# Optimization experiments

Measured on AMD Instinct MI355X. Metric: run time of the kernel, lower is better.

## Reference

```python
import jax, jax.numpy as jnp
import numpy as np

T, B, S, D = 128, 32, 100, 256  # targetL, batch, sourceL, output_size
EPS = 1e-6

def setup_inputs() -> dict:
    key = jax.random.key(0)
    ks = jax.random.split(key, 9)
    sc = 0.05  # weight init scale
    inp = {
        'prev_layer': jax.random.normal(ks[0], (T, B, D), dtype=jnp.float32),
        'hidden': jax.random.normal(ks[1], (B, D), dtype=jnp.float32),
        'enc_output': jax.random.normal(ks[2], (T * B, S, D), dtype=jnp.float32),
        # linear weights (layer_norm=True -> no biases on linears)
        'W_in': jax.random.normal(ks[3], (D, 3 * D), dtype=jnp.float32) * sc,
        'W_hid': jax.random.normal(ks[4], (D, D), dtype=jnp.float32) * sc,
        'W_ctx': jax.random.normal(ks[5], (D, D), dtype=jnp.float32) * sc,
        'W_enc': jax.random.normal(ks[6], (D, D), dtype=jnp.float32) * sc,
        'W_q': jax.random.normal(ks[7], (D, D), dtype=jnp.float32) * sc,   # MLPAttention query proj
        'v_att': jax.random.normal(ks[8], (D,), dtype=jnp.float32) * sc,  # MLPAttention score vector
        # layernorm affine params
        'g_pre': jnp.ones(3 * D, jnp.float32), 'b_pre': jnp.zeros(3 * D, jnp.float32),
        'g_enc': jnp.ones(D, jnp.float32), 'b_enc': jnp.zeros(D, jnp.float32),
        'g_h': jnp.ones(D, jnp.float32), 'b_h': jnp.zeros(D, jnp.float32),
        'g_c': jnp.ones(D, jnp.float32), 'b_c': jnp.zeros(D, jnp.float32),
        'g_q': jnp.ones(D, jnp.float32), 'b_q': jnp.zeros(D, jnp.float32),
    }
    return inp

def _ln(x, g, b):
    m = jnp.mean(x, axis=-1, keepdims=True)
    v = jnp.mean((x - m) ** 2, axis=-1, keepdims=True)
    return g * (x - m) / jnp.sqrt(v + EPS) + b

def reference(prev_layer, hidden, enc_output, W_in, W_hid, W_ctx, W_enc, W_q, v_att,
              g_pre, b_pre, g_enc, b_enc, g_h, b_h, g_c, b_c, g_q, b_q):
    Tl, Bb, Dd = prev_layer.shape
    # input / encoder projections (dropout=0 -> identity)
    preact = _ln(prev_layer @ W_in, g_pre, b_pre)        # [T,B,3D]
    pctx = _ln(enc_output @ W_enc, g_enc, b_enc)         # [T*B,S,D]
    z, h_gate, x_t = jnp.split(preact, 3, axis=-1)
    z = jax.nn.sigmoid(z)
    h_gate = jax.nn.sigmoid(h_gate)
    # SRU-style elementwise linear recurrence over time
    def step(h, zx):
        zt, xt = zx
        s = (1.0 - zt) * h + zt * xt
        return s, s
    final_h, ss = jax.lax.scan(step, hidden, (z, x_t))   # ss: [T,B,D]
    # MLP (Bahdanau) attention: scores = v . tanh(LN(Wq s) + pctx)
    q = _ln(ss @ W_q, g_q, b_q).reshape(Tl * Bb, 1, Dd)
    scores = jnp.einsum('nsd,d->ns', jnp.tanh(q + pctx), v_att)  # [T*B,S]
    attn = jax.nn.softmax(scores, axis=-1)
    attn_out = jnp.einsum('ns,nsd->nd', attn, pctx).reshape(Tl, Bb, Dd)
    attn_out = attn_out / np.sqrt(Dd).astype(np.float32)
    out = jnp.tanh(_ln(ss @ W_hid, g_h, b_h) + _ln(attn_out @ W_ctx, g_c, b_c))
    out = (1.0 - h_gate) * out + h_gate * prev_layer     # highway gate
    return out, final_h, attn
```

## Files before the change

### kernel.cpp

```cpp
#include <hip/hip_runtime.h>
#include <hip/hip_bf16.h>
#include <math.h>

typedef short  s16x8 __attribute__((ext_vector_type(8)));
typedef float  f32x4 __attribute__((ext_vector_type(4)));
typedef float  f32x2 __attribute__((ext_vector_type(2)));

#define LN_EPS 1e-6f

__device__ __forceinline__ unsigned short f2bf(float x) {
  union { float f; unsigned u; } v; v.f = x;
  unsigned r = v.u + 0x7FFFu + ((v.u >> 16) & 1u);
  return (unsigned short)(r >> 16);
}
__device__ __forceinline__ float bf2f(unsigned short u) {
  union { unsigned u; float f; } v; v.u = ((unsigned)u) << 16;
  return v.f;
}
__device__ __forceinline__ float bflo(unsigned u) {
  union { unsigned u; float f; } v; v.u = u << 16; return v.f;
}
__device__ __forceinline__ float bfhi(unsigned u) {
  union { unsigned u; float f; } v; v.u = u & 0xFFFF0000u; return v.f;
}
__device__ __forceinline__ unsigned pack_bf2(float a, float b) {
  __hip_bfloat162 h = __float22bfloat162_rn(make_float2(a, b));
  unsigned u; __builtin_memcpy(&u, &h, 4); return u;
}
__device__ __forceinline__ float fast_tanh(float x) {
  float e = __expf(2.0f * x);
  return 1.0f - 2.0f * __builtin_amdgcn_rcpf(e + 1.0f);
}
__device__ __forceinline__ float fast_sigmoid(float x) {
  return __builtin_amdgcn_rcpf(1.0f + __expf(-x));
}

__device__ __forceinline__ float wredsum(float v) {
  #pragma unroll
  for (int m = 32; m >= 1; m >>= 1) v += __shfl_xor(v, m);
  return v;
}

__device__ __forceinline__ f32x4 mfma16(s16x8 a, s16x8 b, f32x4 c) {
  return __builtin_amdgcn_mfma_f32_16x16x32_bf16(a, b, c, 0, 0, 0);
}

__device__ __forceinline__ void stage_rows(unsigned short* A, const float* src,
                                           int rows, int tid, int nthreads) {
  char* Ab = (char*)A;
  int nquads = rows * 64;
  for (int p = tid; p < nquads; p += nthreads) {
    int row = p >> 6, kq = p & 63;
    f32x4 v = *(const f32x4*)(src + row * 256 + kq * 4);
    unsigned u0 = pack_bf2(v.x, v.y);
    unsigned u1 = pack_bf2(v.z, v.w);
    int byte = row * 512 + ((kq * 8) ^ ((row & 7) << 4));
    *(uint2*)(Ab + byte) = uint2{u0, u1};
  }
}

__device__ __forceinline__ s16x8 readA(const unsigned short* A, int row, int kk, int hi) {
  const char* Ab = (const char*)A;
  int byte = row * 512 + (((kk * 64) + hi * 16) ^ ((row & 7) << 4));
  return *(const s16x8*)(Ab + byte);
}
__device__ __forceinline__ s16x8 readB(const unsigned short* Bt, int col, int kk, int hi) {
  return *(const s16x8*)(Bt + col * 256 + kk * 32 + hi * 8);
}

__global__ __launch_bounds__(256) void k_convw(
    const float* Win, const float* Wq, const float* Whid, const float* Wctx, const float* Wenc,
    unsigned short* bt_in, unsigned short* bt_q, unsigned short* bt_hid,
    unsigned short* bt_ctx, unsigned short* bt_enc) {
  int e = blockIdx.x * 256 + threadIdx.x;
  if (e < 196608) {
    int k = e & 255, n = e >> 8;
    bt_in[n * 256 + k] = f2bf(Win[k * 768 + n]);
    return;
  }
  e -= 196608;
  int m = e >> 16;
  int r = e & 65535;
  int k = r & 255, n = r >> 8;
  const float* src = (m == 0) ? Wq : (m == 1) ? Whid : (m == 2) ? Wctx : Wenc;
  unsigned short* dst = (m == 0) ? bt_q : (m == 1) ? bt_hid : (m == 2) ? bt_ctx : bt_enc;
  dst[n * 256 + k] = f2bf(src[k * 256 + n]);
}

__global__ __launch_bounds__(256) void k_preact(
    const float* prev, const unsigned short* bt_in,
    const float* g_pre, const float* b_pre,
    float* Z, float* HG, float* XT) {
  __shared__ __align__(16) unsigned short A[16 * 256];
  __shared__ float C[16 * 768];
  int tid = threadIdx.x, lane = tid & 63, wave = tid >> 6;
  int hi = lane >> 4, lo = lane & 15;
  int r0 = blockIdx.x * 16;
  stage_rows(A, prev + (size_t)r0 * 256, 16, tid, 256);
  __syncthreads();
  f32x4 acc[12];
  #pragma unroll
  for (int ct = 0; ct < 12; ct++) acc[ct] = f32x4{0.f, 0.f, 0.f, 0.f};
  #pragma unroll
  for (int kk = 0; kk < 8; kk++) {
    s16x8 a = readA(A, lo, kk, hi);
    #pragma unroll
    for (int ct = 0; ct < 12; ct++) {
      s16x8 b = readB(bt_in, wave * 192 + ct * 16 + lo, kk, hi);
      acc[ct] = mfma16(a, b, acc[ct]);
    }
  }
  #pragma unroll
  for (int ct = 0; ct < 12; ct++) {
    int col = wave * 192 + ct * 16 + lo;
    #pragma unroll
    for (int r = 0; r < 4; r++) C[(hi * 4 + r) * 768 + col] = acc[ct][r];
  }
  __syncthreads();
  #pragma unroll
  for (int mm = 0; mm < 4; mm++) {
    int m = wave * 4 + mm;
    float x[12]; float s = 0.f, q = 0.f;
    #pragma unroll
    for (int i = 0; i < 12; i++) {
      x[i] = C[m * 768 + lane + 64 * i];
      s += x[i]; q += x[i] * x[i];
    }
    s = wredsum(s); q = wredsum(q);
    float mean = s * (1.0f / 768.0f);
    float var = q * (1.0f / 768.0f) - mean * mean;
    float rstd = rsqrtf(var + LN_EPS);
    int gr = r0 + m;
    #pragma unroll
    for (int i = 0; i < 12; i++) {
      int c = lane + 64 * i;
      float y = g_pre[c] * (x[i] - mean) * rstd + b_pre[c];
      if (c < 256)      Z [gr * 256 + c]         = fast_sigmoid(y);
      else if (c < 512) HG[gr * 256 + (c - 256)] = fast_sigmoid(y);
      else              XT[gr * 256 + (c - 512)] = y;
    }
  }
}

__global__ __launch_bounds__(256) void k_scan(
    const float* hidden, const float* Z, const float* XT,
    float* SS, float* outFinalH) {
  int tid = blockIdx.x * 256 + threadIdx.x;
  float h = hidden[tid];
  for (int t0 = 0; t0 < 128; t0 += 8) {
    float zc[8], xc[8];
    #pragma unroll
    for (int j = 0; j < 8; j++) {
      zc[j] = Z [(t0 + j) * 8192 + tid];
      xc[j] = XT[(t0 + j) * 8192 + tid];
    }
    #pragma unroll
    for (int j = 0; j < 8; j++) {
      h = (1.0f - zc[j]) * h + zc[j] * xc[j];
      SS[(t0 + j) * 8192 + tid] = h;
    }
  }
  outFinalH[tid] = h;
}

__global__ __launch_bounds__(256) void k_qproj(
    const float* SS, const unsigned short* bt_q,
    const float* g_q, const float* b_q, float* Q) {
  __shared__ __align__(16) unsigned short A[16 * 256];
  __shared__ float C[16 * 256];
  int tid = threadIdx.x, lane = tid & 63, wave = tid >> 6;
  int hi = lane >> 4, lo = lane & 15;
  int r0 = blockIdx.x * 16;
  stage_rows(A, SS + (size_t)r0 * 256, 16, tid, 256);
  __syncthreads();
  f32x4 acc[4];
  #pragma unroll
  for (int ct = 0; ct < 4; ct++) acc[ct] = f32x4{0.f, 0.f, 0.f, 0.f};
  #pragma unroll
  for (int kk = 0; kk < 8; kk++) {
    s16x8 a = readA(A, lo, kk, hi);
    #pragma unroll
    for (int ct = 0; ct < 4; ct++) {
      s16x8 b = readB(bt_q, wave * 64 + ct * 16 + lo, kk, hi);
      acc[ct] = mfma16(a, b, acc[ct]);
    }
  }
  #pragma unroll
  for (int ct = 0; ct < 4; ct++) {
    int col = wave * 64 + ct * 16 + lo;
    #pragma unroll
    for (int r = 0; r < 4; r++) C[(hi * 4 + r) * 256 + col] = acc[ct][r];
  }
  __syncthreads();
  #pragma unroll
  for (int mm = 0; mm < 4; mm++) {
    int m = wave * 4 + mm;
    float x[4]; float s = 0.f, q = 0.f;
    #pragma unroll
    for (int i = 0; i < 4; i++) {
      x[i] = C[m * 256 + lane + 64 * i];
      s += x[i]; q += x[i] * x[i];
    }
    s = wredsum(s); q = wredsum(q);
    float mean = s * (1.0f / 256.0f);
    float var = q * (1.0f / 256.0f) - mean * mean;
    float rstd = rsqrtf(var + LN_EPS);
    int gr = r0 + m;
    #pragma unroll
    for (int i = 0; i < 4; i++) {
      int c = lane + 64 * i;
      Q[gr * 256 + c] = g_q[c] * (x[i] - mean) * rstd + b_q[c];
    }
  }
}

__global__ __launch_bounds__(512) void k_attn(
    const float* enc, const unsigned short* bt_enc, const float* Q,
    const float* g_enc, const float* b_enc, const float* v_att,
    float* AOUT, float* attnOut) {
  __shared__ __align__(16) unsigned short AP[112 * 256];
  __shared__ float scores[112];
  __shared__ float beta_s;
  __shared__ float qs[256], gs[256], bs[256], vs[256];
  float*  means = (float*) ((char*)AP + 55296);
  float*  rstds = (float*) ((char*)AP + 55744);
  f32x2*  part  = (f32x2*) ((char*)AP + 51200);
  int n = blockIdx.x;
  int tid = threadIdx.x, lane = tid & 63, wave = tid >> 6;
  int hi = lane >> 4, lo = lane & 15;
  if (tid < 256) {
    qs[tid] = Q[n * 256 + tid];
    gs[tid] = g_enc[tid]; bs[tid] = b_enc[tid]; vs[tid] = v_att[tid];
  }
  stage_rows(AP, enc + (size_t)n * 25600, 100, tid, 512);
  __syncthreads();
  f32x4 acc[7][2];
  #pragma unroll
  for (int mt = 0; mt < 7; mt++) {
    acc[mt][0] = f32x4{0.f, 0.f, 0.f, 0.f};
    acc[mt][1] = f32x4{0.f, 0.f, 0.f, 0.f};
  }
  #pragma unroll
  for (int kk = 0; kk < 8; kk++) {
    s16x8 b0 = readB(bt_enc, wave * 32 + lo, kk, hi);
    s16x8 b1 = readB(bt_enc, wave * 32 + 16 + lo, kk, hi);
    #pragma unroll
    for (int mt = 0; mt < 7; mt++) {
      s16x8 a = readA(AP, mt * 16 + lo, kk, hi);
      acc[mt][0] = mfma16(a, b0, acc[mt][0]);
      acc[mt][1] = mfma16(a, b1, acc[mt][1]);
    }
  }
  __syncthreads();
  #pragma unroll
  for (int mt = 0; mt < 7; mt++) {
    #pragma unroll
    for (int ct = 0; ct < 2; ct++) {
      int col = wave * 32 + ct * 16 + lo;
      #pragma unroll
      for (int r = 0; r < 4; r++) {
        int row = mt * 16 + hi * 4 + r;
        if (row < 100) AP[row * 256 + col] = f2bf(acc[mt][ct][r]);
      }
    }
  }
  __syncthreads();
  {
    int ca = lane * 2;
    float g0 = gs[ca], g1 = gs[ca + 1], g2 = gs[ca + 128], g3 = gs[ca + 129];
    float b0 = bs[ca], b1 = bs[ca + 1], b2 = bs[ca + 128], b3 = bs[ca + 129];
    float v0 = vs[ca], v1 = vs[ca + 1], v2 = vs[ca + 128], v3 = vs[ca + 129];
    float q0 = qs[ca], q1 = qs[ca + 1], q2 = qs[ca + 128], q3 = qs[ca + 129];
    for (int m = wave; m < 100; m += 8) {
      const unsigned* Prow = (const unsigned*)(AP + m * 256);
      unsigned u01 = Prow[lane], u23 = Prow[lane + 64];
      float x0 = bflo(u01), x1 = bfhi(u01), x2 = bflo(u23), x3 = bfhi(u23);
      float s = (x0 + x1) + (x2 + x3);
      float q = fmaf(x0, x0, fmaf(x1, x1, fmaf(x2, x2, x3 * x3)));
      s = wredsum(s); q = wredsum(q);
      float mean = s * (1.0f / 256.0f);
      float var = q * (1.0f / 256.0f) - mean * mean;
      float rstd = rsqrtf(var + LN_EPS);
      float sc;
      sc  = v0 * fast_tanh(q0 + fmaf(g0, (x0 - mean) * rstd, b0));
      sc += v1 * fast_tanh(q1 + fmaf(g1, (x1 - mean) * rstd, b1));
      sc += v2 * fast_tanh(q2 + fmaf(g2, (x2 - mean) * rstd, b2));
      sc += v3 * fast_tanh(q3 + fmaf(g3, (x3 - mean) * rstd, b3));
      sc = wredsum(sc);
      if (lane == 0) { scores[m] = sc; means[m] = mean; rstds[m] = rstd; }
    }
  }
  __syncthreads();
  if (wave == 0) {
    float s1 = (lane < 100) ? scores[lane] : -INFINITY;
    float s2 = (lane + 64 < 100) ? scores[lane + 64] : -INFINITY;
    float mx = fmaxf(s1, s2);
    #pragma unroll
    for (int m = 32; m >= 1; m >>= 1) mx = fmaxf(mx, __shfl_xor(mx, m));
    float e1 = (lane < 100) ? __expf(s1 - mx) : 0.f;
    float e2 = (lane + 64 < 100) ? __expf(s2 - mx) : 0.f;
    float sm = wredsum(e1 + e2);
    float inv = __builtin_amdgcn_rcpf(sm);
    float p1 = e1 * inv, p2 = e2 * inv;
    float r1 = (lane < 100) ? rstds[lane] : 0.f;
    float m1 = (lane < 100) ? means[lane] : 0.f;
    float r2 = (lane + 64 < 100) ? rstds[lane + 64] : 0.f;
    float m2 = (lane + 64 < 100) ? means[lane + 64] : 0.f;
    scores[lane] = p1 * r1;
    if (lane + 64 < 112) scores[lane + 64] = p2 * r2;
    float bp = wredsum(fmaf(p1 * r1, m1, p2 * r2 * m2));
    if (lane == 0) beta_s = bp;
    if (lane < 100) attnOut[(size_t)n * 100 + lane] = p1;
    if (lane + 64 < 100) attnOut[(size_t)n * 100 + lane + 64] = p2;
  }
  __syncthreads();
  {
    int cp = tid & 127, h = tid >> 7;
    float a0 = 0.f, a1 = 0.f;
    #pragma unroll 5
    for (int s = h * 25; s < h * 25 + 25; s++) {
      unsigned u = *(const unsigned*)(AP + s * 256 + cp * 2);
      float al = scores[s];
      a0 = fmaf(al, bflo(u), a0);
      a1 = fmaf(al, bfhi(u), a1);
    }
    part[h * 128 + cp] = f32x2{a0, a1};
  }
  __syncthreads();
  if (tid < 256) {
    const float* pf = (const float*)part;
    int idx = (tid >> 1) * 2 + (tid & 1);
    float S1 = pf[idx] + pf[256 + idx] + pf[512 + idx] + pf[768 + idx];
    float y = fmaf(gs[tid], S1 - beta_s, bs[tid]);
    AOUT[(size_t)n * 256 + tid] = y * 0.0625f;
  }
}

__global__ __launch_bounds__(256) void k_out(
    const float* SS, const float* AOUT,
    const unsigned short* bt_hid, const unsigned short* bt_ctx,
    const float* g_h, const float* b_h, const float* g_c, const float* b_c,
    const float* HG, const float* prev, float* out) {
  __shared__ __align__(16) unsigned short A1[16 * 256];
  __shared__ __align__(16) unsigned short A2[16 * 256];
  __shared__ float C1[16 * 256];
  __shared__ float C2[16 * 256];
  int tid = threadIdx.x, lane = tid & 63, wave = tid >> 6;
  int hi = lane >> 4, lo = lane & 15;
  int r0 = blockIdx.x * 16;
  stage_rows(A1, SS + (size_t)r0 * 256, 16, tid, 256);
  stage_rows(A2, AOUT + (size_t)r0 * 256, 16, tid, 256);
  __syncthreads();
  f32x4 acc1[4], acc2[4];
  #pragma unroll
  for (int ct = 0; ct < 4; ct++) {
    acc1[ct] = f32x4{0.f, 0.f, 0.f, 0.f};
    acc2[ct] = f32x4{0.f, 0.f, 0.f, 0.f};
  }
  #pragma unroll
  for (int kk = 0; kk < 8; kk++) {
    s16x8 a1 = readA(A1, lo, kk, hi);
    s16x8 a2 = readA(A2, lo, kk, hi);
    #pragma unroll
    for (int ct = 0; ct < 4; ct++) {
      int col = wave * 64 + ct * 16 + lo;
      s16x8 b1 = readB(bt_hid, col, kk, hi);
      s16x8 b2 = readB(bt_ctx, col, kk, hi);
      acc1[ct] = mfma16(a1, b1, acc1[ct]);
      acc2[ct] = mfma16(a2, b2, acc2[ct]);
    }
  }
  #pragma unroll
  for (int ct = 0; ct < 4; ct++) {
    int col = wave * 64 + ct * 16 + lo;
    #pragma unroll
    for (int r = 0; r < 4; r++) {
      C1[(hi * 4 + r) * 256 + col] = acc1[ct][r];
      C2[(hi * 4 + r) * 256 + col] = acc2[ct][r];
    }
  }
  __syncthreads();
  #pragma unroll
  for (int mm = 0; mm < 4; mm++) {
    int m = wave * 4 + mm;
    float x1[4], x2[4];
    float s1 = 0.f, q1 = 0.f, s2 = 0.f, q2 = 0.f;
    #pragma unroll
    for (int i = 0; i < 4; i++) {
      x1[i] = C1[m * 256 + lane + 64 * i];
      x2[i] = C2[m * 256 + lane + 64 * i];
      s1 += x1[i]; q1 += x1[i] * x1[i];
      s2 += x2[i]; q2 += x2[i] * x2[i];
    }
    s1 = wredsum(s1); q1 = wredsum(q1);
    s2 = wredsum(s2); q2 = wredsum(q2);
    float mean1 = s1 * (1.0f / 256.0f), var1 = q1 * (1.0f / 256.0f) - mean1 * mean1;
    float mean2 = s2 * (1.0f / 256.0f), var2 = q2 * (1.0f / 256.0f) - mean2 * mean2;
    float rstd1 = rsqrtf(var1 + LN_EPS), rstd2 = rsqrtf(var2 + LN_EPS);
    int gr = r0 + m;
    #pragma unroll
    for (int i = 0; i < 4; i++) {
      int c = lane + 64 * i;
      float y1 = g_h[c] * (x1[i] - mean1) * rstd1 + b_h[c];
      float y2 = g_c[c] * (x2[i] - mean2) * rstd2 + b_c[c];
      float y = fast_tanh(y1 + y2);
      float g = HG[gr * 256 + c];
      float pv = prev[gr * 256 + c];
      out[gr * 256 + c] = (1.0f - g) * y + g * pv;
    }
  }
}

extern "C" void kernel_launch(void* const* d_in, const int* in_sizes, int n_in,
                              void* d_out, int out_size, void* d_ws, size_t ws_size,
                              hipStream_t stream) {
  const float* prev   = (const float*)d_in[0];
  const float* hidden = (const float*)d_in[1];
  const float* enc    = (const float*)d_in[2];
  const float* W_in   = (const float*)d_in[3];
  const float* W_hid  = (const float*)d_in[4];
  const float* W_ctx  = (const float*)d_in[5];
  const float* W_enc  = (const float*)d_in[6];
  const float* W_q    = (const float*)d_in[7];
  const float* v_att  = (const float*)d_in[8];
  const float* g_pre  = (const float*)d_in[9];
  const float* b_pre  = (const float*)d_in[10];
  const float* g_enc  = (const float*)d_in[11];
  const float* b_enc  = (const float*)d_in[12];
  const float* g_h    = (const float*)d_in[13];
  const float* b_h    = (const float*)d_in[14];
  const float* g_c    = (const float*)d_in[15];
  const float* b_c    = (const float*)d_in[16];
  const float* g_q    = (const float*)d_in[17];
  const float* b_q    = (const float*)d_in[18];

  char* ws = (char*)d_ws;
  unsigned short* BT_IN  = (unsigned short*)(ws + 0);
  unsigned short* BT_Q   = (unsigned short*)(ws + 393216);
  unsigned short* BT_HID = (unsigned short*)(ws + 524288);
  unsigned short* BT_CTX = (unsigned short*)(ws + 655360);
  unsigned short* BT_ENC = (unsigned short*)(ws + 786432);
  float* Z    = (float*)(ws + 917504);
  float* HG   = (float*)(ws + 5111808);
  float* XT   = (float*)(ws + 9306112);
  float* SS   = (float*)(ws + 13500416);
  float* Q    = (float*)(ws + 17694720);
  float* AOUT = (float*)(ws + 21889024);

  float* out    = (float*)d_out;
  float* finalH = out + 1048576;
  float* attnO  = out + 1056768;

  k_convw <<<1792, 256, 0, stream>>>(W_in, W_q, W_hid, W_ctx, W_enc,
                                     BT_IN, BT_Q, BT_HID, BT_CTX, BT_ENC);
  k_preact<<<256, 256, 0, stream>>>(prev, BT_IN, g_pre, b_pre, Z, HG, XT);
  k_scan  <<<32, 256, 0, stream>>>(hidden, Z, XT, SS, finalH);
  k_qproj <<<256, 256, 0, stream>>>(SS, BT_Q, g_q, b_q, Q);
  k_attn  <<<4096, 512, 0, stream>>>(enc, BT_ENC, Q, g_enc, b_enc, v_att, AOUT, attnO);
  k_out   <<<256, 256, 0, stream>>>(SS, AOUT, BT_HID, BT_CTX,
                                    g_h, b_h, g_c, b_c, HG, prev, out);
}
```

Measured before the change: 307.7 us.

## Shrink attention LDS, use DPP reductions, tile weight transpose conversion

Several changes land at once. The attention kernel's shared memory is cut from about 60KB to about 52KB by dropping the q/g/b/v staging arrays (those values are now read directly from global) and by reusing a small stat buffer, and launch bounds now request 6 waves per SIMD. Wave reductions move from shuffles to DPP row operations plus readlane. The weight-conversion kernel becomes a 32x32 LDS-tiled transpose with coalesced reads and writes. The weighted-sum phase drops from four partial groups to two, with a clamped A-row index. The aim is higher occupancy in the dominant attention kernel and less shuffle and LDS overhead, at the risk of register pressure from the bound and some duplicate reads of row 99.

```diff
diff --git a/kernel.cpp b/kernel.cpp
--- a/kernel.cpp
+++ b/kernel.cpp
@@ -35,10 +35,43 @@
   return __builtin_amdgcn_rcpf(1.0f + __expf(-x));
 }
 
+template <int CTRL>
+__device__ __forceinline__ float dpp_add(float v) {
+  union { float f; int i; } a, r;
+  a.f = v;
+  r.i = __builtin_amdgcn_update_dpp(0, a.i, CTRL, 0xF, 0xF, true);
+  return v + r.f;
+}
+template <int CTRL>
+__device__ __forceinline__ float dpp_max(float v) {
+  union { float f; int i; } a, r;
+  a.f = v;
+  r.i = __builtin_amdgcn_update_dpp(a.i, a.i, CTRL, 0xF, 0xF, false);
+  return fmaxf(v, r.f);
+}
+__device__ __forceinline__ float bcast63(float v) {
+  union { float f; int i; } a, r;
+  a.f = v;
+  r.i = __builtin_amdgcn_readlane(a.i, 63);
+  return r.f;
+}
 __device__ __forceinline__ float wredsum(float v) {
-  #pragma unroll
-  for (int m = 32; m >= 1; m >>= 1) v += __shfl_xor(v, m);
-  return v;
+  v = dpp_add<0x128>(v);
+  v = dpp_add<0x124>(v);
+  v = dpp_add<0x122>(v);
+  v = dpp_add<0x121>(v);
+  v = dpp_add<0x142>(v);
+  v = dpp_add<0x143>(v);
+  return bcast63(v);
+}
+__device__ __forceinline__ float wredmax(float v) {
+  v = dpp_max<0x128>(v);
+  v = dpp_max<0x124>(v);
+  v = dpp_max<0x122>(v);
+  v = dpp_max<0x121>(v);
+  v = dpp_max<0x142>(v);
+  v = dpp_max<0x143>(v);
+  return bcast63(v);
 }
 
 __device__ __forceinline__ f32x4 mfma16(s16x8 a, s16x8 b, f32x4 c) {
@@ -49,6 +82,7 @@
                                            int rows, int tid, int nthreads) {
   char* Ab = (char*)A;
   int nquads = rows * 64;
+  #pragma unroll 4
   for (int p = tid; p < nquads; p += nthreads) {
     int row = p >> 6, kq = p & 63;
     f32x4 v = *(const f32x4*)(src + row * 256 + kq * 4);
@@ -72,19 +106,30 @@
     const float* Win, const float* Wq, const float* Whid, const float* Wctx, const float* Wenc,
     unsigned short* bt_in, unsigned short* bt_q, unsigned short* bt_hid,
     unsigned short* bt_ctx, unsigned short* bt_enc) {
-  int e = blockIdx.x * 256 + threadIdx.x;
-  if (e < 196608) {
-    int k = e & 255, n = e >> 8;
-    bt_in[n * 256 + k] = f2bf(Win[k * 768 + n]);
-    return;
-  }
-  e -= 196608;
-  int m = e >> 16;
-  int r = e & 65535;
-  int k = r & 255, n = r >> 8;
-  const float* src = (m == 0) ? Wq : (m == 1) ? Whid : (m == 2) ? Wctx : Wenc;
-  unsigned short* dst = (m == 0) ? bt_q : (m == 1) ? bt_hid : (m == 2) ? bt_ctx : bt_enc;
-  dst[n * 256 + k] = f2bf(src[k * 256 + n]);
+  __shared__ unsigned short tile[32][34];
+  int b = blockIdx.x;
+  const float* src; unsigned short* dst; int N, tk, tn;
+  if (b < 192) { src = Win; dst = bt_in; N = 768; tk = b & 7; tn = b >> 3; }
+  else {
+    int bb = b - 192; int m = bb >> 6; int r = bb & 63;
+    tk = r & 7; tn = r >> 3; N = 256;
+    src = (m == 0) ? Wq : (m == 1) ? Whid : (m == 2) ? Wctx : Wenc;
+    dst = (m == 0) ? bt_q : (m == 1) ? bt_hid : (m == 2) ? bt_ctx : bt_enc;
+  }
+  int k0 = tk * 32, n0 = tn * 32;
+  {
+    int i = threadIdx.x >> 3, j4 = (threadIdx.x & 7) * 4;
+    f32x4 v = *(const f32x4*)(src + (size_t)(k0 + i) * N + n0 + j4);
+    *(unsigned*)((char*)&tile[i][j4])     = pack_bf2(v.x, v.y);
+    *(unsigned*)((char*)&tile[i][j4 + 2]) = pack_bf2(v.z, v.w);
+  }
+  __syncthreads();
+  {
+    int j = threadIdx.x >> 3, i4 = (threadIdx.x & 7) * 4;
+    unsigned lo = (unsigned)tile[i4 + 0][j] | ((unsigned)tile[i4 + 1][j] << 16);
+    unsigned hi = (unsigned)tile[i4 + 2][j] | ((unsigned)tile[i4 + 3][j] << 16);
+    *(uint2*)(dst + (size_t)(n0 + j) * 256 + k0 + i4) = uint2{lo, hi};
+  }
 }
 
 __global__ __launch_bounds__(256) void k_preact(
@@ -214,24 +259,17 @@
   }
 }
 
-__global__ __launch_bounds__(512) void k_attn(
+__global__ __launch_bounds__(512, 6) void k_attn(
     const float* enc, const unsigned short* bt_enc, const float* Q,
     const float* g_enc, const float* b_enc, const float* v_att,
     float* AOUT, float* attnOut) {
-  __shared__ __align__(16) unsigned short AP[112 * 256];
-  __shared__ float scores[112];
+  __shared__ __align__(16) unsigned short AP[100 * 256];
+  __shared__ __align__(16) float alpha[112];
+  __shared__ __align__(16) float stat[256];
   __shared__ float beta_s;
-  __shared__ float qs[256], gs[256], bs[256], vs[256];
-  float*  means = (float*) ((char*)AP + 55296);
-  float*  rstds = (float*) ((char*)AP + 55744);
-  f32x2*  part  = (f32x2*) ((char*)AP + 51200);
   int n = blockIdx.x;
   int tid = threadIdx.x, lane = tid & 63, wave = tid >> 6;
   int hi = lane >> 4, lo = lane & 15;
-  if (tid < 256) {
-    qs[tid] = Q[n * 256 + tid];
-    gs[tid] = g_enc[tid]; bs[tid] = b_enc[tid]; vs[tid] = v_att[tid];
-  }
   stage_rows(AP, enc + (size_t)n * 25600, 100, tid, 512);
   __syncthreads();
   f32x4 acc[7][2];
@@ -246,7 +284,9 @@
     s16x8 b1 = readB(bt_enc, wave * 32 + 16 + lo, kk, hi);
     #pragma unroll
     for (int mt = 0; mt < 7; mt++) {
-      s16x8 a = readA(AP, mt * 16 + lo, kk, hi);
+      int ar = mt * 16 + lo;
+      ar = ar > 99 ? 99 : ar;
+      s16x8 a = readA(AP, ar, kk, hi);
       acc[mt][0] = mfma16(a, b0, acc[mt][0]);
       acc[mt][1] = mfma16(a, b1, acc[mt][1]);
     }
@@ -254,23 +294,26 @@
   __syncthreads();
   #pragma unroll
   for (int mt = 0; mt < 7; mt++) {
-    #pragma unroll
-    for (int ct = 0; ct < 2; ct++) {
-      int col = wave * 32 + ct * 16 + lo;
-      #pragma unroll
-      for (int r = 0; r < 4; r++) {
-        int row = mt * 16 + hi * 4 + r;
-        if (row < 100) AP[row * 256 + col] = f2bf(acc[mt][ct][r]);
+    int col = wave * 32 + lo;
+    #pragma unroll
+    for (int r = 0; r < 4; r++) {
+      int row = mt * 16 + hi * 4 + r;
+      if (row < 100) {
+        unsigned u = pack_bf2(acc[mt][0][r], acc[mt][1][r]);
+        AP[row * 256 + col]      = (unsigned short)u;
+        AP[row * 256 + col + 16] = (unsigned short)(u >> 16);
       }
     }
   }
   __syncthreads();
   {
     int ca = lane * 2;
-    float g0 = gs[ca], g1 = gs[ca + 1], g2 = gs[ca + 128], g3 = gs[ca + 129];
-    float b0 = bs[ca], b1 = bs[ca + 1], b2 = bs[ca + 128], b3 = bs[ca + 129];
-    float v0 = vs[ca], v1 = vs[ca + 1], v2 = vs[ca + 128], v3 = vs[ca + 129];
-    float q0 = qs[ca], q1 = qs[ca + 1], q2 = qs[ca + 128], q3 = qs[ca + 129];
+    f32x2 gA = *(const f32x2*)(g_enc + ca), gB = *(const f32x2*)(g_enc + ca + 128);
+    f32x2 bA = *(const f32x2*)(b_enc + ca), bB = *(const f32x2*)(b_enc + ca + 128);
+    f32x2 vA = *(const f32x2*)(v_att + ca), vB = *(const f32x2*)(v_att + ca + 128);
+    f32x2 qA = *(const f32x2*)(Q + (size_t)n * 256 + ca);
+    f32x2 qB = *(const f32x2*)(Q + (size_t)n * 256 + ca + 128);
+    #pragma unroll 2
     for (int m = wave; m < 100; m += 8) {
       const unsigned* Prow = (const unsigned*)(AP + m * 256);
       unsigned u01 = Prow[lane], u23 = Prow[lane + 64];
@@ -282,57 +325,53 @@
       float var = q * (1.0f / 256.0f) - mean * mean;
       float rstd = rsqrtf(var + LN_EPS);
       float sc;
-      sc  = v0 * fast_tanh(q0 + fmaf(g0, (x0 - mean) * rstd, b0));
-      sc += v1 * fast_tanh(q1 + fmaf(g1, (x1 - mean) * rstd, b1));
-      sc += v2 * fast_tanh(q2 + fmaf(g2, (x2 - mean) * rstd, b2));
-      sc += v3 * fast_tanh(q3 + fmaf(g3, (x3 - mean) * rstd, b3));
+      sc  = vA.x * fast_tanh(qA.x + fmaf(gA.x, (x0 - mean) * rstd, bA.x));
+      sc += vA.y * fast_tanh(qA.y + fmaf(gA.y, (x1 - mean) * rstd, bA.y));
+      sc += vB.x * fast_tanh(qB.x + fmaf(gB.x, (x2 - mean) * rstd, bB.x));
+      sc += vB.y * fast_tanh(qB.y + fmaf(gB.y, (x3 - mean) * rstd, bB.y));
       sc = wredsum(sc);
-      if (lane == 0) { scores[m] = sc; means[m] = mean; rstds[m] = rstd; }
+      if (lane == 0) { alpha[m] = sc; stat[m] = mean; stat[112 + m] = rstd; }
     }
   }
   __syncthreads();
   if (wave == 0) {
-    float s1 = (lane < 100) ? scores[lane] : -INFINITY;
-    float s2 = (lane + 64 < 100) ? scores[lane + 64] : -INFINITY;
-    float mx = fmaxf(s1, s2);
-    #pragma unroll
-    for (int m = 32; m >= 1; m >>= 1) mx = fmaxf(mx, __shfl_xor(mx, m));
+    float s1 = (lane < 100) ? alpha[lane] : -INFINITY;
+    float s2 = (lane < 36)  ? alpha[lane + 64] : -INFINITY;
+    float mx = wredmax(fmaxf(s1, s2));
     float e1 = (lane < 100) ? __expf(s1 - mx) : 0.f;
-    float e2 = (lane + 64 < 100) ? __expf(s2 - mx) : 0.f;
+    float e2 = (lane < 36)  ? __expf(s2 - mx) : 0.f;
     float sm = wredsum(e1 + e2);
     float inv = __builtin_amdgcn_rcpf(sm);
     float p1 = e1 * inv, p2 = e2 * inv;
-    float r1 = (lane < 100) ? rstds[lane] : 0.f;
-    float m1 = (lane < 100) ? means[lane] : 0.f;
-    float r2 = (lane + 64 < 100) ? rstds[lane + 64] : 0.f;
-    float m2 = (lane + 64 < 100) ? means[lane + 64] : 0.f;
-    scores[lane] = p1 * r1;
-    if (lane + 64 < 112) scores[lane + 64] = p2 * r2;
-    float bp = wredsum(fmaf(p1 * r1, m1, p2 * r2 * m2));
+    float r1 = (lane < 100) ? stat[112 + lane] : 0.f;
+    float m1 = (lane < 100) ? stat[lane] : 0.f;
+    float r2 = (lane < 36)  ? stat[112 + lane + 64] : 0.f;
+    float m2 = (lane < 36)  ? stat[lane + 64] : 0.f;
+    float a1 = p1 * r1, a2 = p2 * r2;
+    alpha[lane] = a1;
+    if (lane < 48) alpha[lane + 64] = a2;
+    float bp = wredsum(fmaf(a1, m1, a2 * m2));
     if (lane == 0) beta_s = bp;
     if (lane < 100) attnOut[(size_t)n * 100 + lane] = p1;
-    if (lane + 64 < 100) attnOut[(size_t)n * 100 + lane + 64] = p2;
+    if (lane < 36)  attnOut[(size_t)n * 100 + lane + 64] = p2;
   }
   __syncthreads();
   {
-    int cp = tid & 127, h = tid >> 7;
-    float a0 = 0.f, a1 = 0.f;
+    int c = tid & 255, h = tid >> 8;
+    float a = 0.f;
     #pragma unroll 5
-    for (int s = h * 25; s < h * 25 + 25; s++) {
-      unsigned u = *(const unsigned*)(AP + s * 256 + cp * 2);
-      float al = scores[s];
-      a0 = fmaf(al, bflo(u), a0);
-      a1 = fmaf(al, bfhi(u), a1);
-    }
-    part[h * 128 + cp] = f32x2{a0, a1};
-  }
-  __syncthreads();
-  if (tid < 256) {
-    const float* pf = (const float*)part;
-    int idx = (tid >> 1) * 2 + (tid & 1);
-    float S1 = pf[idx] + pf[256 + idx] + pf[512 + idx] + pf[768 + idx];
-    float y = fmaf(gs[tid], S1 - beta_s, bs[tid]);
-    AOUT[(size_t)n * 256 + tid] = y * 0.0625f;
+    for (int s = h * 50; s < h * 50 + 50; s += 2) {
+      f32x2 al = *(const f32x2*)(alpha + s);
+      a = fmaf(al.x, bf2f(AP[s * 256 + c]), a);
+      a = fmaf(al.y, bf2f(AP[(s + 1) * 256 + c]), a);
+    }
+    if (h == 1) stat[c] = a;
+    __syncthreads();
+    if (h == 0) {
+      float S1 = a + stat[c];
+      float y = fmaf(g_enc[c], S1 - beta_s, b_enc[c]);
+      AOUT[(size_t)n * 256 + c] = y * 0.0625f;
+    }
   }
 }
 
@@ -451,8 +490,8 @@
   float* finalH = out + 1048576;
   float* attnO  = out + 1056768;
 
-  k_convw <<<1792, 256, 0, stream>>>(W_in, W_q, W_hid, W_ctx, W_enc,
-                                     BT_IN, BT_Q, BT_HID, BT_CTX, BT_ENC);
+  k_convw <<<448, 256, 0, stream>>>(W_in, W_q, W_hid, W_ctx, W_enc,
+                                    BT_IN, BT_Q, BT_HID, BT_CTX, BT_ENC);
   k_preact<<<256, 256, 0, stream>>>(prev, BT_IN, g_pre, b_pre, Z, HG, XT);
   k_scan  <<<32, 256, 0, stream>>>(hidden, Z, XT, SS, finalH);
   k_qproj <<<256, 256, 0, stream>>>(SS, BT_Q, g_q, b_q, Q);
```

Result: faster. 289.5 us (-5.9%).
